# Optimization experiments

Hardware: AMD Instinct MI355X
Metric: run time of the kernel (lower is better)

## Reference

```python
import jax, jax.numpy as jnp
import numpy as np

MASK_VALUE = 0.0

def setup_inputs() -> dict:
    key = jax.random.key(0)
    k1, k2, k3 = jax.random.split(key, 3)
    B, N, F, K = 8, 10000, 64, 8
    inp = jax.random.normal(k1, (B, N, F), dtype=jnp.float32)
    inds = jax.random.randint(k2, (B, N, K), 0, N, dtype=jnp.int32)
    # sprinkle some negative (masked) indices, like padded neighbor slots
    neg = jax.random.uniform(k3, (B, N, K)) < 0.1
    inds = jnp.where(neg, jnp.int32(-1), inds)
    return {"inp": inp, "inds": inds}

def reference(inp, inds):
    B, N, F = inp.shape
    K = inds.shape[-1]
    inp_p = inp.reshape(-1, F)                      # [B*N, F]
    inds_p = inds.reshape(-1, K)                    # [B*N, K]
    # which sequence each flat row belongs to, offset into flat node table
    seq_offset = (jnp.arange(inds_p.shape[0], dtype=jnp.int32) // N) * N
    mask = inds_p >= 0
    # wrap local index by N (faithful to tf.mod), add per-sequence offset
    offset = jnp.where(mask, (inds_p % N) + seq_offset[:, None],
                       jnp.int32(B * N))            # masked -> sentinel row
    # append mask-value row so sentinel index gathers mask_value features
    table = jnp.concatenate(
        [inp_p, jnp.full((1, F), MASK_VALUE, dtype=inp.dtype)], axis=0)
    neighb = table[offset]                          # [B*N, K, F] gather
    neighb = neighb.reshape(B, N, K, F)
    # include_self: concat self features as extra neighbor slot
    out = jnp.concatenate([neighb, inp[:, :, None, :]], axis=2)  # [B,N,K+1,F]
    return out
```

## Files before the change

kernel.cpp:

```cpp
#include <hip/hip_runtime.h>


constexpr int B   = 8;
constexpr int N   = 10000;
constexpr int F   = 64;
constexpr int K   = 8;
constexpr int KP1 = K + 1;
constexpr int ROWS = B * N * KP1;

__global__ __launch_bounds__(256)
void GatherFromIndices_kernel(const float* __restrict__ inp,
                              const int*   __restrict__ inds,
                              float*       __restrict__ out) {
    int t    = blockIdx.x * 256 + threadIdx.x;
    int r    = t >> 4;
    int lane = t & 15;

    if (r >= ROWS) return;

    int k  = r % KP1;
    int bn = r / KP1;

    float4 v;
    if (k == K) {
        v = ((const float4*)(inp + (size_t)bn * F))[lane];
    } else {
        int idx = inds[bn * K + k];
        if (idx < 0) {
            v = make_float4(0.f, 0.f, 0.f, 0.f);
        } else {
            int b   = bn / N;
            int row = b * N + (idx % N);
            v = ((const float4*)(inp + (size_t)row * F))[lane];
        }
    }
    ((float4*)out)[(size_t)r * 16 + lane] = v;
}

extern "C" void kernel_launch(void* const* d_in, const int* in_sizes, int n_in,
                              void* d_out, int out_size, void* d_ws, size_t ws_size,
                              hipStream_t stream) {
    const float* inp  = (const float*)d_in[0];
    const int*   inds = (const int*)d_in[1];
    float*       out  = (float*)d_out;

    int total_threads = ROWS * 16;
    int blocks = (total_threads + 255) / 256;
    GatherFromIndices_kernel<<<blocks, 256, 0, stream>>>(inp, inds, out);
}
```

Before: 222.6 us.

## Process all neighbor slots per node in one thread group with vectorized index loads

Each 16-lane group now handles one node and loops over all K+1 output slots, loading the node's 8 indices with two int4 loads instead of one scalar index load per row. Blocks are interleaved across batches so that concurrently running blocks touch different batch tables. This removes per-row div/mod arithmetic and redundant index loads, and gives each thread several independent loads in flight. It relies on N being divisible by 16 and launches far fewer threads, so fewer waves are available to hide gather latency.

```diff
diff --git a/kernel.cpp b/kernel.cpp
--- a/kernel.cpp
+++ b/kernel.cpp
@@ -1,40 +1,48 @@
 #include <hip/hip_runtime.h>
 
+
+typedef float f32x4 __attribute__((ext_vector_type(4)));
+typedef int   i32x4 __attribute__((ext_vector_type(4)));
 
 constexpr int B   = 8;
 constexpr int N   = 10000;
 constexpr int F   = 64;
 constexpr int K   = 8;
 constexpr int KP1 = K + 1;
-constexpr int ROWS = B * N * KP1;
+constexpr int GROUPS_PER_BLOCK = 16;
+constexpr int BLOCKS_PER_BATCH = N / GROUPS_PER_BLOCK;
+constexpr int NBLOCKS = BLOCKS_PER_BATCH * B;
 
 __global__ __launch_bounds__(256)
 void GatherFromIndices_kernel(const float* __restrict__ inp,
                               const int*   __restrict__ inds,
                               float*       __restrict__ out) {
-    int t    = blockIdx.x * 256 + threadIdx.x;
-    int r    = t >> 4;
-    int lane = t & 15;
+    int b    = blockIdx.x & 7;
+    int slot = blockIdx.x >> 3;
+    int g    = threadIdx.x >> 4;
+    int lane = threadIdx.x & 15;
 
-    if (r >= ROWS) return;
+    int n  = slot * GROUPS_PER_BLOCK + g;
+    int bn = b * N + n;
 
-    int k  = r % KP1;
-    int bn = r / KP1;
+    const i32x4* ip = (const i32x4*)(inds + (size_t)bn * K);
+    i32x4 i0 = ip[0];
+    i32x4 i1 = ip[1];
 
-    float4 v;
-    if (k == K) {
-        v = ((const float4*)(inp + (size_t)bn * F))[lane];
-    } else {
-        int idx = inds[bn * K + k];
-        if (idx < 0) {
-            v = make_float4(0.f, 0.f, 0.f, 0.f);
-        } else {
-            int b   = bn / N;
-            int row = b * N + (idx % N);
-            v = ((const float4*)(inp + (size_t)row * F))[lane];
+    const f32x4* table = (const f32x4*)inp;
+    f32x4* outp = (f32x4*)out + (size_t)bn * (KP1 * 16) + lane;
+
+#pragma unroll
+    for (int k = 0; k < K; ++k) {
+        int iv = (k < 4) ? i0[k] : i1[k - 4];
+        f32x4 v = (f32x4){0.f, 0.f, 0.f, 0.f};
+        if (iv >= 0) {
+            int row = b * N + (iv % N);
+            v = table[(size_t)row * 16 + lane];
         }
+        outp[k * 16] = v;
     }
-    ((float4*)out)[(size_t)r * 16 + lane] = v;
+    outp[K * 16] = table[(size_t)bn * 16 + lane];
 }
 
 extern "C" void kernel_launch(void* const* d_in, const int* in_sizes, int n_in,
@@ -44,7 +52,5 @@
     const int*   inds = (const int*)d_in[1];
     float*       out  = (float*)d_out;
 
-    int total_threads = ROWS * 16;
-    int blocks = (total_threads + 255) / 256;
-    GatherFromIndices_kernel<<<blocks, 256, 0, stream>>>(inp, inds, out);
+    GatherFromIndices_kernel<<<NBLOCKS, 256, 0, stream>>>(inp, inds, out);
 }
```

Result: faster. 206.5 us (-7.2%).
